# Performance work log

Hardware: AMD Instinct MI355X
Metric: run time of the kernel (lower is better)

The kernel has to match this reference:

```python
import jax, jax.numpy as jnp
import numpy as np

THRESH = 1.0
DECAY = 0.5


def setup_inputs() -> dict:
    key = jax.random.key(0)
    X = jax.random.normal(key, (32, 128, 32, 32, 16), dtype=jnp.float32)
    return {"X": X}


def reference(X):
    # Leaky-integrate-and-fire scan over the trailing time axis.
    Xt = jnp.moveaxis(X, -1, 0)  # [T, B, C, H, W] time-leading for scan

    def step(mem, x_t):
        mem = mem * DECAY + x_t                      # leaky integration
        s = (mem >= THRESH).astype(X.dtype)          # threshold spike
        mem = mem * (1.0 - s)                        # hard reset on spike
        return mem, s

    _, spikes = jax.lax.scan(step, jnp.zeros_like(Xt[0]), Xt)
    return jnp.moveaxis(spikes, 0, -1)  # back to [..., T]
```

## Files before the change

kernel.cpp:

```cpp
#include <hip/hip_runtime.h>


#define LIF_DECAY  0.5f
#define LIF_THRESH 1.0f

#define LIF_STEP(v)                                        \
    {                                                      \
        m = m * LIF_DECAY + (v);                           \
        float sp = (m >= LIF_THRESH) ? 1.0f : 0.0f;        \
        (v) = sp;                                          \
        m = (sp != 0.0f) ? 0.0f : m;                       \
    }

__global__ __launch_bounds__(256) void lif_kernel(const float4* __restrict__ X4,
                                                  float4* __restrict__ O4) {
    __shared__ float4 lds[4 * 257];

    const int tid = threadIdx.x;
    const size_t base = (size_t)blockIdx.x * 1024;

    const int q  = tid & 3;
    const int plc = (tid >> 2);

#pragma unroll
    for (int k = 0; k < 4; ++k) {
        float4 v = X4[base + (size_t)(k * 256 + tid)];
        lds[q * 257 + (k * 64 + plc)] = v;
    }
    __syncthreads();

    float4 f0 = lds[0 * 257 + tid];
    float4 f1 = lds[1 * 257 + tid];
    float4 f2 = lds[2 * 257 + tid];
    float4 f3 = lds[3 * 257 + tid];

    float m = 0.0f;
    LIF_STEP(f0.x) LIF_STEP(f0.y) LIF_STEP(f0.z) LIF_STEP(f0.w)
    LIF_STEP(f1.x) LIF_STEP(f1.y) LIF_STEP(f1.z) LIF_STEP(f1.w)
    LIF_STEP(f2.x) LIF_STEP(f2.y) LIF_STEP(f2.z) LIF_STEP(f2.w)
    LIF_STEP(f3.x) LIF_STEP(f3.y) LIF_STEP(f3.z) LIF_STEP(f3.w)

    __syncthreads();

    lds[0 * 257 + tid] = f0;
    lds[1 * 257 + tid] = f1;
    lds[2 * 257 + tid] = f2;
    lds[3 * 257 + tid] = f3;
    __syncthreads();

#pragma unroll
    for (int k = 0; k < 4; ++k) {
        O4[base + (size_t)(k * 256 + tid)] = lds[q * 257 + (k * 64 + plc)];
    }
}

extern "C" void kernel_launch(void* const* d_in, const int* in_sizes, int n_in,
                              void* d_out, int out_size, void* d_ws, size_t ws_size,
                              hipStream_t stream) {
    (void)n_in; (void)d_ws; (void)ws_size; (void)out_size;
    const float4* X4 = (const float4*)d_in[0];
    float4* O4 = (float4*)d_out;

    int n_f4 = in_sizes[0] / 4;
    int grid = n_f4 / 1024;
    lif_kernel<<<grid, 256, 0, stream>>>(X4, O4);
}
```

Measured before the change: 425.9 us.

## Make LDS transpose wave-private and use nontemporal global loads/stores

```diff
diff --git a/kernel.cpp b/kernel.cpp
--- a/kernel.cpp
+++ b/kernel.cpp
@@ -3,6 +3,8 @@
 
 #define LIF_DECAY  0.5f
 #define LIF_THRESH 1.0f
+
+typedef float f4 __attribute__((ext_vector_type(4)));
 
 #define LIF_STEP(v)                                        \
     {                                                      \
@@ -12,27 +14,34 @@
         m = (sp != 0.0f) ? 0.0f : m;                       \
     }
 
-__global__ __launch_bounds__(256) void lif_kernel(const float4* __restrict__ X4,
-                                                  float4* __restrict__ O4) {
-    __shared__ float4 lds[4 * 257];
+__global__ __launch_bounds__(256) void lif_kernel(const f4* __restrict__ X4,
+                                                  f4* __restrict__ O4) {
+    __shared__ f4 lds[4][4 * 65];
 
     const int tid = threadIdx.x;
-    const size_t base = (size_t)blockIdx.x * 1024;
+    const int wv  = tid >> 6;
+    const int l   = tid & 63;
+    const int q   = l & 3;
+    const int p   = l >> 2;
 
-    const int q  = tid & 3;
-    const int plc = (tid >> 2);
+    f4* __restrict__ w_lds = &lds[wv][0];
+    const size_t wbase = (size_t)blockIdx.x * 1024 + (size_t)wv * 256;
 
-#pragma unroll
-    for (int k = 0; k < 4; ++k) {
-        float4 v = X4[base + (size_t)(k * 256 + tid)];
-        lds[q * 257 + (k * 64 + plc)] = v;
-    }
-    __syncthreads();
+    f4 v0 = __builtin_nontemporal_load(&X4[wbase +   0 + l]);
+    f4 v1 = __builtin_nontemporal_load(&X4[wbase +  64 + l]);
+    f4 v2 = __builtin_nontemporal_load(&X4[wbase + 128 + l]);
+    f4 v3 = __builtin_nontemporal_load(&X4[wbase + 192 + l]);
+    w_lds[q * 65 + ( 0 + p)] = v0;
+    w_lds[q * 65 + (16 + p)] = v1;
+    w_lds[q * 65 + (32 + p)] = v2;
+    w_lds[q * 65 + (48 + p)] = v3;
 
-    float4 f0 = lds[0 * 257 + tid];
-    float4 f1 = lds[1 * 257 + tid];
-    float4 f2 = lds[2 * 257 + tid];
-    float4 f3 = lds[3 * 257 + tid];
+    asm volatile("s_waitcnt lgkmcnt(0)" ::: "memory");
+
+    f4 f0 = w_lds[0 * 65 + l];
+    f4 f1 = w_lds[1 * 65 + l];
+    f4 f2 = w_lds[2 * 65 + l];
+    f4 f3 = w_lds[3 * 65 + l];
 
     float m = 0.0f;
     LIF_STEP(f0.x) LIF_STEP(f0.y) LIF_STEP(f0.z) LIF_STEP(f0.w)
@@ -40,26 +49,25 @@
     LIF_STEP(f2.x) LIF_STEP(f2.y) LIF_STEP(f2.z) LIF_STEP(f2.w)
     LIF_STEP(f3.x) LIF_STEP(f3.y) LIF_STEP(f3.z) LIF_STEP(f3.w)
 
-    __syncthreads();
+    w_lds[0 * 65 + l] = f0;
+    w_lds[1 * 65 + l] = f1;
+    w_lds[2 * 65 + l] = f2;
+    w_lds[3 * 65 + l] = f3;
 
-    lds[0 * 257 + tid] = f0;
-    lds[1 * 257 + tid] = f1;
-    lds[2 * 257 + tid] = f2;
-    lds[3 * 257 + tid] = f3;
-    __syncthreads();
+    asm volatile("s_waitcnt lgkmcnt(0)" ::: "memory");
 
-#pragma unroll
-    for (int k = 0; k < 4; ++k) {
-        O4[base + (size_t)(k * 256 + tid)] = lds[q * 257 + (k * 64 + plc)];
-    }
+    __builtin_nontemporal_store(w_lds[q * 65 + ( 0 + p)], &O4[wbase +   0 + l]);
+    __builtin_nontemporal_store(w_lds[q * 65 + (16 + p)], &O4[wbase +  64 + l]);
+    __builtin_nontemporal_store(w_lds[q * 65 + (32 + p)], &O4[wbase + 128 + l]);
+    __builtin_nontemporal_store(w_lds[q * 65 + (48 + p)], &O4[wbase + 192 + l]);
 }
 
 extern "C" void kernel_launch(void* const* d_in, const int* in_sizes, int n_in,
                               void* d_out, int out_size, void* d_ws, size_t ws_size,
                               hipStream_t stream) {
     (void)n_in; (void)d_ws; (void)ws_size; (void)out_size;
-    const float4* X4 = (const float4*)d_in[0];
-    float4* O4 = (float4*)d_out;
+    const f4* X4 = (const f4*)d_in[0];
+    f4* O4 = (f4*)d_out;
 
     int n_f4 = in_sizes[0] / 4;
     int grid = n_f4 / 1024;
```

New measurement: 413.9 us. -2.8%, faster.
